# Kernel tuning notes

Measured on AMD Instinct MI355X. Metric: run time of the kernel, lower is better.

## Reference

```python
import jax, jax.numpy as jnp
import numpy as np

B, N, M = 4, 1024, 2048
D, H, HD, L, V = 768, 6, 128, 3, 4096
PEH = 64
FF = 4 * D
TEMP0 = 15.5


def _rms(x, w):
    return x * jax.lax.rsqrt(jnp.mean(x * x, axis=-1, keepdims=True) + 1e-8) * w


def _l2(x):
    n = jnp.sqrt(jnp.sum(x * x, axis=-1, keepdims=True))
    return x / jnp.maximum(n, 1e-12)


def setup_inputs():
    key = jax.random.key(0)
    it = iter(jax.random.split(key, 32))

    def rn(shape, s=0.02):
        return jax.random.normal(next(it), shape, jnp.float32) * s

    inp = {}
    inp['tokens'] = jax.random.randint(next(it), (B, N), 0, V)
    inp['acoustic'] = jax.random.normal(next(it), (B, M, D), jnp.float32)
    inp['embed'] = rn((V, D))
    inp['pe_freq'] = rn((PEH // 2,), 1.0)
    inp['pe_w'] = rn((PEH, D))
    inp['pe_b'] = jnp.zeros((D,), jnp.float32)
    inp['dpb_w0'] = rn((1, 64), 0.5)
    inp['dpb_b0'] = jnp.zeros((64,), jnp.float32)
    inp['dpb_w1'] = rn((64, 64), 0.1)
    inp['dpb_b1'] = jnp.zeros((64,), jnp.float32)
    inp['dpb_w2'] = rn((64, H), 0.1)
    inp['dpb_b2'] = jnp.zeros((H,), jnp.float32)
    inp['acoustic_norm_w'] = jnp.ones((D,), jnp.float32)
    inp['norm1'] = jnp.ones((L, D), jnp.float32)
    inp['norm2'] = jnp.ones((L, D), jnp.float32)
    inp['norm3'] = jnp.ones((L, D), jnp.float32)
    inp['sa_qkv'] = rn((L, D, 3 * H * HD))
    inp['sa_out'] = rn((L, H * HD, D))
    inp['temp'] = jnp.full((L,), TEMP0, jnp.float32)
    inp['ca_q'] = rn((L, D, H * HD))
    inp['ca_kv'] = rn((L, D, 2 * H * HD))
    inp['ca_out'] = rn((L, H * HD, D))
    inp['ff_w1'] = rn((L, D, FF))
    inp['ff_w2'] = rn((L, FF, D))
    inp['final_norm_w'] = jnp.ones((D,), jnp.float32)
    inp['out_w'] = rn((D, V))
    inp['out_b'] = jnp.zeros((V,), jnp.float32)
    return inp


def reference(tokens, acoustic, embed, pe_freq, pe_w, pe_b, dpb_w0, dpb_b0, dpb_w1, dpb_b1, dpb_w2, dpb_b2, acoustic_norm_w, norm1, norm2, norm3, sa_qkv, sa_out, temp, ca_q, ca_kv, ca_out, ff_w1, ff_w2, final_norm_w, out_w, out_b):
    x = embed[tokens]  # [B,N,D]
    # learnable fourier positional encoding (hidden_dim=64)
    p = jnp.arange(N, dtype=jnp.float32)[:, None]
    feat = jnp.concatenate([jnp.cos(p * pe_freq), jnp.sin(p * pe_freq)], axis=-1) / jnp.sqrt(jnp.float32(PEH))
    x = x + (feat @ pe_w + pe_b)

    # DynamicPositionBias: MLP over relative distance -> [H,N,N]
    dist = jnp.arange(-(N - 1), N, dtype=jnp.float32)[:, None]  # [2N-1,1]
    hmlp = jax.nn.silu(dist @ dpb_w0 + dpb_b0)
    hmlp = jax.nn.silu(hmlp @ dpb_w1 + dpb_b1)
    table = hmlp @ dpb_w2 + dpb_b2  # [2N-1, H]
    i = jnp.arange(N)
    rel = i[None, :] - i[:, None] + (N - 1)  # [N,N]
    pos_bias = jnp.transpose(table[rel], (2, 0, 1))  # [H,N,N]
    causal = i[None, :] > i[:, None]  # True where key index > query index
    neg = -jnp.finfo(jnp.float32).max

    xkv = _rms(acoustic, acoustic_norm_w)  # acoustic_norm applied once

    for l in range(L):
        # --- cosine-sim causal self-attention with temperature + pos bias ---
        hx = _rms(x, norm1[l])
        qkv = (hx @ sa_qkv[l]).reshape(B, N, H, HD, 3)  # 'b n (h d qkv)'
        q = jnp.transpose(qkv[..., 0], (0, 2, 1, 3))  # [B,H,N,HD]
        k = jnp.transpose(qkv[..., 1], (0, 2, 1, 3))
        v = jnp.transpose(qkv[..., 2], (0, 2, 1, 3))
        q, k = _l2(q), _l2(k)
        dots = jnp.einsum('bhid,bhjd->bhij', q, k) * temp[l] + pos_bias
        dots = jnp.where(causal, neg, dots)
        attn = jax.nn.softmax(dots, axis=-1)
        o = jnp.einsum('bhij,bhjd->bhid', attn, v)
        o = jnp.transpose(o, (0, 2, 1, 3)).reshape(B, N, H * HD)
        x = x + o @ sa_out[l]

        # --- cross attention to acoustic features (flash-attn math, scale 1/sqrt(d)) ---
        hx = _rms(x, norm2[l])
        q = (hx @ ca_q[l]).reshape(B, N, H, HD)
        kv = (xkv @ ca_kv[l]).reshape(B, M, H, HD, 2)  # 'b n (h d kv)'
        k, v = kv[..., 0], kv[..., 1]
        dots = jnp.einsum('bihd,bjhd->bhij', q, k) / jnp.sqrt(jnp.float32(HD))
        attn = jax.nn.softmax(dots, axis=-1)
        o = jnp.einsum('bhij,bjhd->bihd', attn, v).reshape(B, N, H * HD)
        x = x + o @ ca_out[l]

        # --- feed-forward: linear -> gelu -> linear ---
        hx = _rms(x, norm3[l])
        x = x + jax.nn.gelu(hx @ ff_w1[l], approximate=True) @ ff_w2[l]

    logits = _rms(x, final_norm_w) @ out_w + out_b  # [B,N,V]
    return logits
```

## Files before the change

kernel.cpp:

```cpp
#include <hip/hip_runtime.h>
#include <hip/hip_bf16.h>
#include <math.h>
#include <stddef.h>

#define Bc 4
#define Nc 1024
#define Mc 2048
#define Dc 768
#define Hc 6
#define HDc 128
#define Lc 3
#define Vc 4096
#define FFc 3072

typedef short bf16x8 __attribute__((ext_vector_type(8)));
typedef float f32x4 __attribute__((ext_vector_type(4)));
typedef ushort usx4 __attribute__((ext_vector_type(4)));

__device__ __forceinline__ float gelu_tanh(float x) {
    float x3 = x * x * x;
    return 0.5f * x * (1.0f + tanhf(0.7978845608028654f * (x + 0.044715f * x3)));
}
__device__ __forceinline__ float silu_f(float x) {
    return x / (1.0f + expf(-x));
}
__device__ __forceinline__ ushort f2bf(float x) {
    unsigned u = __float_as_uint(x);
    unsigned r = (u + 0x7fffu + ((u >> 16) & 1u)) >> 16;
    return (ushort)r;
}
__device__ __forceinline__ float bf2f(ushort u) {
    return __uint_as_float(((unsigned)u) << 16);
}
__device__ __forceinline__ void gl2lds16(const ushort* g, ushort* l) {
    __builtin_amdgcn_global_load_lds(
        (const __attribute__((address_space(1))) unsigned int*)(g),
        (__attribute__((address_space(3))) unsigned int*)(l),
        16, 0, 0);
}
__device__ __forceinline__ int xcd_swz(int bid, int nwg) {
    int q = nwg >> 3, r = nwg & 7;
    int xcd = bid & 7, i = bid >> 3;
    return (xcd < r ? xcd * (q + 1) : r * (q + 1) + (xcd - r) * q) + i;
}

__global__ __launch_bounds__(256) void pos_pe_kernel(
    const float* __restrict__ freq, const float* __restrict__ pe_w,
    const float* __restrict__ pe_b, float* __restrict__ pos)
{
    int n = blockIdx.x;
    __shared__ float feat[64];
    int tid = threadIdx.x;
    if (tid < 64) {
        float f;
        if (tid < 32) f = cosf((float)n * freq[tid]);
        else          f = sinf((float)n * freq[tid - 32]);
        feat[tid] = f * 0.125f;
    }
    __syncthreads();
    for (int d = tid; d < Dc; d += 256) {
        float s = pe_b[d];
#pragma unroll
        for (int h = 0; h < 64; ++h) s += feat[h] * pe_w[h * Dc + d];
        pos[(size_t)n * Dc + d] = s;
    }
}

__global__ __launch_bounds__(256) void embed_kernel(
    const int* __restrict__ tokens, const float* __restrict__ embed_w,
    const float* __restrict__ pos, float* __restrict__ x)
{
    size_t idx = (size_t)blockIdx.x * 256 + threadIdx.x;
    if (idx >= (size_t)Bc * Nc * Dc) return;
    int d  = (int)(idx % Dc);
    size_t bn = idx / Dc;
    int n  = (int)(bn % Nc);
    int tok = tokens[bn];
    x[idx] = embed_w[(size_t)tok * Dc + d] + pos[(size_t)n * Dc + d];
}

__global__ __launch_bounds__(64) void dpb_kernel(
    const float* __restrict__ w0, const float* __restrict__ b0,
    const float* __restrict__ w1, const float* __restrict__ b1,
    const float* __restrict__ w2, const float* __restrict__ b2,
    float* __restrict__ table)
{
    int r = blockIdx.x;
    int j = threadIdx.x;
    float dist = (float)r - (float)(Nc - 1);
    __shared__ float s0[64], s1[64];
    s0[j] = silu_f(dist * w0[j] + b0[j]);
    __syncthreads();
    float a = b1[j];
#pragma unroll 8
    for (int k = 0; k < 64; ++k) a += s0[k] * w1[k * 64 + j];
    s1[j] = silu_f(a);
    __syncthreads();
    if (j < Hc) {
        float t = b2[j];
#pragma unroll 8
        for (int k = 0; k < 64; ++k) t += s1[k] * w2[k * Hc + j];
        table[(size_t)r * Hc + j] = t;
    }
}

__global__ __launch_bounds__(256) void rms_kernel(
    const float* __restrict__ in, const float* __restrict__ w,
    ushort* __restrict__ out)
{
    size_t row = blockIdx.x;
    const float* rp = in + row * Dc;
    ushort* op = out + row * Dc;
    int tid = threadIdx.x;
    float4 v = make_float4(0.f, 0.f, 0.f, 0.f);
    float s = 0.f;
    int d4 = tid << 2;
    if (tid < 192) {
        v = *(const float4*)&rp[d4];
        s = v.x * v.x + v.y * v.y + v.z * v.z + v.w * v.w;
    }
    __shared__ float red[256];
    red[tid] = s;
    __syncthreads();
    for (int o = 128; o > 0; o >>= 1) {
        if (tid < o) red[tid] += red[tid + o];
        __syncthreads();
    }
    float rs = rsqrtf(red[0] * (1.0f / Dc) + 1e-8f);
    if (tid < 192) {
        float4 wv = *(const float4*)&w[d4];
        usx4 pk;
        pk.x = f2bf(v.x * rs * wv.x); pk.y = f2bf(v.y * rs * wv.y);
        pk.z = f2bf(v.z * rs * wv.z); pk.w = f2bf(v.w * rs * wv.w);
        *(usx4*)&op[d4] = pk;
    }
}

__global__ __launch_bounds__(256) void rms_reduce_kernel(
    float* __restrict__ x, const float* __restrict__ P, int nsplit, size_t MN,
    const float* __restrict__ w, ushort* __restrict__ out)
{
    size_t row = blockIdx.x;
    float* xp = x + row * Dc;
    ushort* op = out + row * Dc;
    int tid = threadIdx.x;
    int d4 = tid << 2;
    float4 v = make_float4(0.f, 0.f, 0.f, 0.f);
    float s = 0.f;
    if (tid < 192) {
        v = *(const float4*)&xp[d4];
        for (int z = 0; z < nsplit; ++z) {
            float4 p = *(const float4*)&P[(size_t)z * MN + row * Dc + d4];
            v.x += p.x; v.y += p.y; v.z += p.z; v.w += p.w;
        }
        *(float4*)&xp[d4] = v;
        s = v.x * v.x + v.y * v.y + v.z * v.z + v.w * v.w;
    }
    __shared__ float red[256];
    red[tid] = s;
    __syncthreads();
    for (int o = 128; o > 0; o >>= 1) {
        if (tid < o) red[tid] += red[tid + o];
        __syncthreads();
    }
    float rs = rsqrtf(red[0] * (1.0f / Dc) + 1e-8f);
    if (tid < 192) {
        float4 wv = *(const float4*)&w[d4];
        usx4 pk;
        pk.x = f2bf(v.x * rs * wv.x); pk.y = f2bf(v.y * rs * wv.y);
        pk.z = f2bf(v.z * rs * wv.z); pk.w = f2bf(v.w * rs * wv.w);
        *(usx4*)&op[d4] = pk;
    }
}

__global__ __launch_bounds__(256) void wt_kernel(
    const float* __restrict__ in, ushort* __restrict__ out, int K_, int N_)
{
    int n0 = blockIdx.x << 6, k0 = blockIdx.y << 6;
    __shared__ ushort t[64][65];
    int tid = threadIdx.x;
    int r = tid >> 4, c4 = (tid & 15) << 2;
    for (int rr = r; rr < 64; rr += 16) {
        float4 v = *(const float4*)&in[(size_t)(k0 + rr) * N_ + n0 + c4];
        t[rr][c4]     = f2bf(v.x);
        t[rr][c4 + 1] = f2bf(v.y);
        t[rr][c4 + 2] = f2bf(v.z);
        t[rr][c4 + 3] = f2bf(v.w);
    }
    __syncthreads();
    int nr = tid >> 2, cw = (tid & 3) << 4;
    ushort tmp[16];
#pragma unroll
    for (int j = 0; j < 16; ++j) tmp[j] = t[cw + j][nr];
#pragma unroll
    for (int s = 0; s < 2; ++s)
        *(bf16x8*)&out[(size_t)(n0 + nr) * K_ + k0 + cw + (s << 3)] =
            *(const bf16x8*)&tmp[s << 3];
}

__global__ __launch_bounds__(512) void gemm_bf16_kernel(
    const ushort* __restrict__ A, const ushort* __restrict__ Bt,
    const float* __restrict__ bias, const float* __restrict__ res,
    float* __restrict__ Cf, ushort* __restrict__ Cb,
    int M_, int N_, int K_, int act, int ksplit)
{
    __shared__ __align__(16) ushort sraw[2 * 2 * 8 * 512];
    ushort* As = sraw;
    ushort* Bs = sraw + 2 * 8 * 512;

    int nwg = gridDim.x * gridDim.y;
    int swz = xcd_swz(blockIdx.y * gridDim.x + blockIdx.x, nwg);
    int n0 = (swz % gridDim.x) << 7;
    int m0 = (swz / gridDim.x) << 7;

    int tid = threadIdx.x;
    int wave = tid >> 6, lane = tid & 63;
    int li = lane & 15, lq = lane >> 4;
    int wm = (wave >> 2) << 6;
    int wn = (wave & 3) << 5;

    int kchunk = K_ / ksplit;
    int kbeg = blockIdx.z * kchunk;
    int niter = kchunk >> 5;

    f32x4 acc[4][2];
#pragma unroll
    for (int i = 0; i < 4; ++i)
#pragma unroll
        for (int j = 0; j < 2; ++j) {
            acc[i][j][0] = 0.f; acc[i][j][1] = 0.f;
            acc[i][j][2] = 0.f; acc[i][j][3] = 0.f;
        }

    auto stage = [&](int buf, int k0) {
        const ushort* ga = A  + (size_t)(m0 + (wave << 4) + li) * K_ + k0 + (lq << 3);
        const ushort* gb = Bt + (size_t)(n0 + (wave << 4) + li) * K_ + k0 + (lq << 3);
        gl2lds16(ga, &As[(buf << 12) + (wave << 9)]);
        gl2lds16(gb, &Bs[(buf << 12) + (wave << 9)]);
    };

    stage(0, kbeg);
    __syncthreads();

    for (int it = 0; it < niter; ++it) {
        int cur = it & 1;
        if (it + 1 < niter) stage(cur ^ 1, kbeg + ((it + 1) << 5));
        bf16x8 af[4], bfr[2];
#pragma unroll
        for (int t = 0; t < 4; ++t)
            af[t]  = *(const bf16x8*)&As[(cur << 12) + (((wm >> 4) + t) << 9) + (lane << 3)];
#pragma unroll
        for (int t = 0; t < 2; ++t)
            bfr[t] = *(const bf16x8*)&Bs[(cur << 12) + (((wn >> 4) + t) << 9) + (lane << 3)];
#pragma unroll
        for (int mt = 0; mt < 4; ++mt)
#pragma unroll
            for (int nt = 0; nt < 2; ++nt)
                acc[mt][nt] = __builtin_amdgcn_mfma_f32_16x16x32_bf16(
                    af[mt], bfr[nt], acc[mt][nt], 0, 0, 0);
        __syncthreads();
    }

    float* lt = (float*)sraw;
    float* dstF = Cf;
    if (ksplit > 1) dstF = Cf + (size_t)blockIdx.z * M_ * N_;

#pragma unroll
    for (int half = 0; half < 2; ++half) {
        __syncthreads();
        if ((wm >> 6) == half) {
#pragma unroll
            for (int mt = 0; mt < 4; ++mt) {
#pragma unroll
                for (int r = 0; r < 4; ++r) {
                    int lrow = (mt << 4) + (lq << 2) + r;
                    int grow = m0 + (half << 6) + lrow;
#pragma unroll
                    for (int nt = 0; nt < 2; ++nt) {
                        int col = wn + (nt << 4) + li;
                        float v = acc[mt][nt][r];
                        if (ksplit == 1) {
                            int gcol = n0 + col;
                            if (bias) v += bias[gcol];
                            if (act == 1) v = gelu_tanh(v);
                            if (res) v += res[(size_t)grow * N_ + gcol];
                        }
                        lt[(lrow << 7) + col] = v;
                    }
                }
            }
        }
        __syncthreads();
        if (Cb) {
            int lrow = tid >> 4;
            int c8 = (tid & 15) << 3;
#pragma unroll
            for (int p = 0; p < 2; ++p) {
                int row = (p << 5) + lrow;
                f32x4 a = *(const f32x4*)&lt[(row << 7) + c8];
                f32x4 b = *(const f32x4*)&lt[(row << 7) + c8 + 4];
                union { bf16x8 v; ushort u[8]; } pk;
#pragma unroll
                for (int j = 0; j < 4; ++j) {
                    pk.u[j] = f2bf(a[j]);
                    pk.u[4 + j] = f2bf(b[j]);
                }
                int grow = m0 + (half << 6) + row;
                *(bf16x8*)&Cb[(size_t)grow * N_ + n0 + c8] = pk.v;
            }
        } else {
            int lrow = tid >> 5;
            int c4 = (tid & 31) << 2;
#pragma unroll
            for (int p = 0; p < 4; ++p) {
                int row = (p << 4) + lrow;
                f32x4 a = *(const f32x4*)&lt[(row << 7) + c4];
                int grow = m0 + (half << 6) + row;
                *(f32x4*)&dstF[(size_t)grow * N_ + n0 + c4] = a;
            }
        }
    }
}

__global__ __launch_bounds__(128) void unpack_sa_kernel(
    const ushort* __restrict__ qkv, ushort* __restrict__ qo,
    ushort* __restrict__ ko, ushort* __restrict__ vo)
{
    int bid = blockIdx.x;
    int h = bid % Hc;
    int bn = bid / Hc;
    int b = bn / Nc, n = bn % Nc;
    int d = threadIdx.x;
    size_t base = (size_t)bn * (3 * Hc * HDc) + (size_t)(h * HDc + d) * 3;
    float q = bf2f(qkv[base]), k = bf2f(qkv[base + 1]);
    ushort v = qkv[base + 2];
    __shared__ float rq[128], rk[128];
    rq[d] = q * q; rk[d] = k * k;
    __syncthreads();
    for (int o = 64; o > 0; o >>= 1) {
        if (d < o) { rq[d] += rq[d + o]; rk[d] += rk[d + o]; }
        __syncthreads();
    }
    float qn = fmaxf(sqrtf(rq[0]), 1e-12f);
    float kn = fmaxf(sqrtf(rk[0]), 1e-12f);
    size_t oidx = (((size_t)(b * Hc + h) * Nc) + n) * HDc + d;
    qo[oidx] = f2bf(q / qn);
    ko[oidx] = f2bf(k / kn);
    vo[oidx] = v;
}

__global__ __launch_bounds__(256) void unpack_caq_red_kernel(
    const float* __restrict__ P, ushort* __restrict__ qo)
{
    size_t idx = (size_t)blockIdx.x * 256 + threadIdx.x;
    if (idx >= (size_t)Bc * Hc * Nc * HDc) return;
    int d = (int)(idx & (HDc - 1));
    size_t t = idx >> 7;
    int n = (int)(t % Nc); t /= Nc;
    int h = (int)(t % Hc); int b = (int)(t / Hc);
    const size_t MNq = (size_t)Bc * Nc * (Hc * HDc);
    size_t src = ((size_t)(b * Nc + n)) * (Hc * HDc) + h * HDc + d;
    qo[idx] = f2bf(P[src] + P[MNq + src]);
}

__global__ __launch_bounds__(256) void unpack_cakv_kernel(
    const ushort* __restrict__ in, ushort* __restrict__ ko, ushort* __restrict__ vo)
{
    size_t idx = (size_t)blockIdx.x * 256 + threadIdx.x;
    if (idx >= (size_t)Bc * Hc * Mc * HDc) return;
    int d = (int)(idx & (HDc - 1));
    size_t t = idx >> 7;
    int m = (int)(t % Mc); t /= Mc;
    int h = (int)(t % Hc); int b = (int)(t / Hc);
    size_t src = ((size_t)(b * Mc + m)) * (2 * Hc * HDc) + (size_t)(h * HDc + d) * 2;
    ko[idx] = in[src];
    vo[idx] = in[src + 1];
}

__global__ __launch_bounds__(256) void transpose_kernel(
    const ushort* __restrict__ in, ushort* __restrict__ out, int R)
{
    int bh = blockIdx.z;
    int r0 = blockIdx.x << 6, d0 = blockIdx.y << 6;
    const ushort* ip = in + (size_t)bh * R * HDc;
    ushort* op = out + (size_t)bh * HDc * R;
    __shared__ ushort tile[64][66];
    int t = threadIdx.x;
    int lr = t >> 5, lc = (t & 31) << 1;
    for (int rr = lr; rr < 64; rr += 8) {
        ushort2 v = *(const ushort2*)&ip[(size_t)(r0 + rr) * HDc + d0 + lc];
        tile[rr][lc] = v.x; tile[rr][lc + 1] = v.y;
    }
    __syncthreads();
    for (int dd = lr; dd < 64; dd += 8) {
        ushort2 v;
        v.x = tile[lc][dd]; v.y = tile[lc + 1][dd];
        *(ushort2*)&op[(size_t)(d0 + dd) * R + r0 + lc] = v;
    }
}

__global__ __launch_bounds__(256) void attn_mfma_kernel(
    const ushort* __restrict__ Qg, const ushort* __restrict__ Kg,
    const ushort* __restrict__ VTg, ushort* __restrict__ O,
    int NQ, int NK, float scale_const, const float* __restrict__ scale_ptr,
    const float* __restrict__ bias_table, int causal)
{
    int qtiles = NQ >> 6;
    int bid = xcd_swz(blockIdx.x, gridDim.x);
    int qt = bid % qtiles;
    int bh = bid / qtiles;
    int h = bh % Hc, b = bh / Hc;
    int q0 = qt << 6;

    const ushort* Qb = Qg + (size_t)bh * NQ * HDc;
    const ushort* Kb = Kg + (size_t)bh * NK * HDc;
    const ushort* Vb = VTg + (size_t)bh * HDc * NK;

    float scale = scale_const * (scale_ptr ? scale_ptr[0] : 1.0f);

    __shared__ __align__(16) ushort Ks[2][16 * 512];
    __shared__ __align__(16) ushort Vs[2][16 * 512];
    __shared__ __align__(16) ushort Ps[4][16][72];
    __shared__ float bias_s[2][128];

    int tid = threadIdx.x;
    int wave = tid >> 6, lane = tid & 63;
    int li = lane & 15, lq = lane >> 4;
    int qrel = (wave << 4) + li;

    bf16x8 qfrag[4];
    {
        const ushort* qrow = Qb + (size_t)(q0 + qrel) * HDc + (lq << 3);
#pragma unroll
        for (int kt = 0; kt < 4; ++kt)
            qfrag[kt] = *(const bf16x8*)&qrow[kt << 5];
    }

    f32x4 oacc[8];
#pragma unroll
    for (int i = 0; i < 8; ++i) { oacc[i][0] = 0.f; oacc[i][1] = 0.f; oacc[i][2] = 0.f; oacc[i][3] = 0.f; }
    float m_run = -INFINITY, l_run = 0.f;

    auto stage_kv = [&](int buf, int jt) {
        int j0 = jt << 6;
#pragma unroll
        for (int i = 0; i < 4; ++i) {
            int f = (wave << 2) + i;
            int mt = f >> 2, kt = f & 3;
            const ushort* gk = Kb + (size_t)(j0 + (mt << 4) + li) * HDc + (kt << 5) + (lq << 3);
            gl2lds16(gk, &Ks[buf][f << 9]);
            int dt = f >> 1, s = f & 1;
            const ushort* gv = Vb + (size_t)((dt << 4) + li) * NK + j0 + (s << 5) + (lq << 3);
            gl2lds16(gv, &Vs[buf][f << 9]);
        }
        if (bias_table && tid < 127)
            bias_s[buf][tid] = bias_table[(size_t)(j0 - q0 - 63 + Nc - 1 + tid) * Hc + h];
    };

    int jt_end = causal ? (q0 >> 6) + 1 : (NK >> 6);

    stage_kv(0, 0);
    __syncthreads();

    for (int jt = 0; jt < jt_end; ++jt) {
        int cur = jt & 1;
        if (jt + 1 < jt_end) stage_kv(cur ^ 1, jt + 1);
        int j0 = jt << 6;

        f32x4 sacc[4];
#pragma unroll
        for (int mt = 0; mt < 4; ++mt) {
            f32x4 s; s[0] = 0.f; s[1] = 0.f; s[2] = 0.f; s[3] = 0.f;
#pragma unroll
            for (int kt = 0; kt < 4; ++kt) {
                bf16x8 kf = *(const bf16x8*)&Ks[cur][(((mt << 2) + kt) << 9) + (lane << 3)];
                s = __builtin_amdgcn_mfma_f32_16x16x32_bf16(kf, qfrag[kt], s, 0, 0, 0);
            }
            sacc[mt] = s;
        }

        float sv[4][4];
        float mtile = -INFINITY;
#pragma unroll
        for (int mt = 0; mt < 4; ++mt)
#pragma unroll
            for (int r = 0; r < 4; ++r) {
                int jrel = (mt << 4) + (lq << 2) + r;
                float sx = sacc[mt][r] * scale;
                if (bias_table) sx += bias_s[cur][jrel - qrel + 63];
                if (causal && (j0 + jrel) > (q0 + qrel)) sx = -INFINITY;
                sv[mt][r] = sx;
                mtile = fmaxf(mtile, sx);
            }
        mtile = fmaxf(mtile, __shfl_xor(mtile, 16));
        mtile = fmaxf(mtile, __shfl_xor(mtile, 32));
        float m_new = fmaxf(m_run, mtile);
        float alpha = __expf(m_run - m_new);
        m_run = m_new;
        float ps = 0.f;
#pragma unroll
        for (int mt = 0; mt < 4; ++mt)
#pragma unroll
            for (int r = 0; r < 4; ++r) {
                float p = __expf(sv[mt][r] - m_new);
                sv[mt][r] = p;
                ps += p;
            }
        ps += __shfl_xor(ps, 16);
        ps += __shfl_xor(ps, 32);
        l_run = l_run * alpha + ps;

#pragma unroll
        for (int mt = 0; mt < 4; ++mt) {
            usx4 pk;
            pk.x = f2bf(sv[mt][0]); pk.y = f2bf(sv[mt][1]);
            pk.z = f2bf(sv[mt][2]); pk.w = f2bf(sv[mt][3]);
            *(usx4*)&Ps[wave][li][(mt << 4) + (lq << 2)] = pk;
        }

        float ar[4];
#pragma unroll
        for (int r = 0; r < 4; ++r) ar[r] = __shfl(alpha, (lq << 2) + r);
#pragma unroll
        for (int dt = 0; dt < 8; ++dt)
#pragma unroll
            for (int r = 0; r < 4; ++r) oacc[dt][r] *= ar[r];

        bf16x8 pf0 = *(const bf16x8*)&Ps[wave][li][(lq << 3)];
        bf16x8 pf1 = *(const bf16x8*)&Ps[wave][li][32 + (lq << 3)];
#pragma unroll
        for (int dt = 0; dt < 8; ++dt) {
            bf16x8 v0 = *(const bf16x8*)&Vs[cur][(((dt << 1) + 0) << 9) + (lane << 3)];
            bf16x8 v1 = *(const bf16x8*)&Vs[cur][(((dt << 1) + 1) << 9) + (lane << 3)];
            oacc[dt] = __builtin_amdgcn_mfma_f32_16x16x32_bf16(pf0, v0, oacc[dt], 0, 0, 0);
            oacc[dt] = __builtin_amdgcn_mfma_f32_16x16x32_bf16(pf1, v1, oacc[dt], 0, 0, 0);
        }
        __syncthreads();
    }

#pragma unroll
    for (int r = 0; r < 4; ++r) {
        float linv = 1.0f / __shfl(l_run, (lq << 2) + r);
        int gq = q0 + (wave << 4) + (lq << 2) + r;
        ushort* op = O + ((size_t)(b * NQ + gq)) * (Hc * HDc) + h * HDc;
#pragma unroll
        for (int dt = 0; dt < 8; ++dt)
            op[(dt << 4) + li] = f2bf(oacc[dt][r] * linv);
    }
}

static inline void launch_gemm(const ushort* A, const ushort* Bt, const float* bias,
                               const float* res, float* Cf, ushort* Cb,
                               int M_, int N_, int K_, int act, int ksplit,
                               hipStream_t s)
{
    dim3 g(N_ / 128, M_ / 128, ksplit);
    hipLaunchKernelGGL(gemm_bf16_kernel, g, dim3(512), 0, s,
                       A, Bt, bias, res, Cf, Cb, M_, N_, K_, act, ksplit);
}

extern "C" void kernel_launch(void* const* d_in, const int* in_sizes, int n_in,
                              void* d_out, int out_size, void* d_ws, size_t ws_size,
                              hipStream_t stream)
{
    const int*   tokens   = (const int*)  d_in[0];
    const float* acoustic = (const float*)d_in[1];
    const float* embed_w  = (const float*)d_in[2];
    const float* pe_freq  = (const float*)d_in[3];
    const float* pe_w     = (const float*)d_in[4];
    const float* pe_b     = (const float*)d_in[5];
    const float* dpb_w0   = (const float*)d_in[6];
    const float* dpb_b0   = (const float*)d_in[7];
    const float* dpb_w1   = (const float*)d_in[8];
    const float* dpb_b1   = (const float*)d_in[9];
    const float* dpb_w2   = (const float*)d_in[10];
    const float* dpb_b2   = (const float*)d_in[11];
    const float* ac_nw    = (const float*)d_in[12];
    const float* norm1    = (const float*)d_in[13];
    const float* norm2    = (const float*)d_in[14];
    const float* norm3    = (const float*)d_in[15];
    const float* sa_qkv   = (const float*)d_in[16];
    const float* sa_out_w = (const float*)d_in[17];
    const float* temp     = (const float*)d_in[18];
    const float* ca_q_w   = (const float*)d_in[19];
    const float* ca_kv_w  = (const float*)d_in[20];
    const float* ca_out_w = (const float*)d_in[21];
    const float* ff_w1    = (const float*)d_in[22];
    const float* ff_w2    = (const float*)d_in[23];
    const float* fin_nw   = (const float*)d_in[24];
    const float* out_w    = (const float*)d_in[25];
    const float* out_b    = (const float*)d_in[26];
    float* out = (float*)d_out;

    const size_t SZ_X   = (size_t)Bc * Nc * Dc;
    const size_t SZ_POS = (size_t)Nc * Dc;
    const size_t SZ_TAB = 16384;
    const size_t SZ_XKV = (size_t)Bc * Mc * Dc;
    const size_t SZ_BIG = (size_t)Bc * Nc * FFc;
    const size_t SZ_QH  = (size_t)Bc * Hc * Nc * HDc;
    const size_t SZ_KH  = (size_t)Bc * Hc * Mc * HDc;

    float* ws = (float*)d_ws;
    float* x     = ws;
    float* pos   = x + SZ_X;
    float* table = pos + SZ_POS;
    ushort* hx    = (ushort*)(table + SZ_TAB);
    ushort* xkvb  = hx + SZ_X;
    ushort* attnO = xkvb + SZ_XKV;
    ushort* bigBb = attnO + SZ_X;
    ushort* qb    = bigBb + SZ_BIG;
    ushort* kb    = qb + SZ_QH;
    ushort* vb    = kb + SZ_KH;
    ushort* vTb   = vb + SZ_KH;
    ushort* wT    = vTb + SZ_KH;

    const size_t W_QKV = (size_t)Dc * 3 * Hc * HDc;
    const size_t W_O   = (size_t)Hc * HDc * Dc;
    const size_t W_CKV = (size_t)Dc * 2 * Hc * HDc;
    const size_t W_F   = (size_t)Dc * FFc;
    const size_t W_LAYER = W_QKV + 3 * W_O + W_CKV + 2 * W_F;
    ushort* outWT = wT + 3 * W_LAYER;

    float* Pq = (float*)qb;
    float* Pk = (float*)kb;
    const size_t MN = (size_t)Bc * Nc * Dc;

    const float CA_SCALE = 0.08838834764831843f;

    for (int l = 0; l < Lc; ++l) {
        ushort* wl = wT + (size_t)l * W_LAYER;
        ushort* qkvT = wl;
        ushort* soT  = qkvT + W_QKV;
        ushort* cqT  = soT + W_O;
        ushort* ckvT = cqT + W_O;
        ushort* coT  = ckvT + W_CKV;
        ushort* f1T  = coT + W_O;
        ushort* f2T  = f1T + W_F;
        hipLaunchKernelGGL(wt_kernel, dim3(3 * Hc * HDc / 64, Dc / 64), dim3(256), 0, stream,
                           sa_qkv + (size_t)l * W_QKV, qkvT, Dc, 3 * Hc * HDc);
        hipLaunchKernelGGL(wt_kernel, dim3(Dc / 64, Hc * HDc / 64), dim3(256), 0, stream,
                           sa_out_w + (size_t)l * W_O, soT, Hc * HDc, Dc);
        hipLaunchKernelGGL(wt_kernel, dim3(Hc * HDc / 64, Dc / 64), dim3(256), 0, stream,
                           ca_q_w + (size_t)l * W_O, cqT, Dc, Hc * HDc);
        hipLaunchKernelGGL(wt_kernel, dim3(2 * Hc * HDc / 64, Dc / 64), dim3(256), 0, stream,
                           ca_kv_w + (size_t)l * W_CKV, ckvT, Dc, 2 * Hc * HDc);
        hipLaunchKernelGGL(wt_kernel, dim3(Dc / 64, Hc * HDc / 64), dim3(256), 0, stream,
                           ca_out_w + (size_t)l * W_O, coT, Hc * HDc, Dc);
        hipLaunchKernelGGL(wt_kernel, dim3(FFc / 64, Dc / 64), dim3(256), 0, stream,
                           ff_w1 + (size_t)l * W_F, f1T, Dc, FFc);
        hipLaunchKernelGGL(wt_kernel, dim3(Dc / 64, FFc / 64), dim3(256), 0, stream,
                           ff_w2 + (size_t)l * W_F, f2T, FFc, Dc);
    }
    hipLaunchKernelGGL(wt_kernel, dim3(Vc / 64, Dc / 64), dim3(256), 0, stream,
                       out_w, outWT, Dc, Vc);

    hipLaunchKernelGGL(pos_pe_kernel, dim3(Nc), dim3(256), 0, stream,
                       pe_freq, pe_w, pe_b, pos);
    hipLaunchKernelGGL(embed_kernel, dim3((unsigned)((SZ_X + 255) / 256)), dim3(256), 0, stream,
                       tokens, embed_w, pos, x);
    hipLaunchKernelGGL(dpb_kernel, dim3(2 * Nc - 1), dim3(64), 0, stream,
                       dpb_w0, dpb_b0, dpb_w1, dpb_b1, dpb_w2, dpb_b2, table);
    hipLaunchKernelGGL(rms_kernel, dim3(Bc * Mc), dim3(256), 0, stream,
                       acoustic, ac_nw, xkvb);

    for (int l = 0; l < Lc; ++l) {
        const float* n1 = norm1 + (size_t)l * Dc;
        const float* n2 = norm2 + (size_t)l * Dc;
        const float* n3 = norm3 + (size_t)l * Dc;
        ushort* wl = wT + (size_t)l * W_LAYER;
        ushort* qkvT = wl;
        ushort* soT  = qkvT + W_QKV;
        ushort* cqT  = soT + W_O;
        ushort* ckvT = cqT + W_O;
        ushort* coT  = ckvT + W_CKV;
        ushort* f1T  = coT + W_O;
        ushort* f2T  = f1T + W_F;

        if (l == 0)
            hipLaunchKernelGGL(rms_kernel, dim3(Bc * Nc), dim3(256), 0, stream, x, n1, hx);
        else
            hipLaunchKernelGGL(rms_reduce_kernel, dim3(Bc * Nc), dim3(256), 0, stream,
                               x, Pq, 3, MN, n1, hx);
        launch_gemm(hx, qkvT, nullptr, nullptr, nullptr, bigBb,
                    Bc * Nc, 3 * Hc * HDc, Dc, 0, 1, stream);
        hipLaunchKernelGGL(unpack_sa_kernel, dim3(Bc * Nc * Hc), dim3(128), 0, stream,
                           bigBb, qb, kb, vb);
        hipLaunchKernelGGL(transpose_kernel, dim3(Nc / 64, 2, Bc * Hc), dim3(256), 0, stream,
                           vb, vTb, Nc);
        hipLaunchKernelGGL(attn_mfma_kernel, dim3(Bc * Hc * (Nc / 64)), dim3(256), 0, stream,
                           qb, kb, vTb, attnO, Nc, Nc, 1.0f, temp + l, table, 1);
        launch_gemm(attnO, soT, nullptr, nullptr, Pq, nullptr,
                    Bc * Nc, Dc, Hc * HDc, 0, 3, stream);
        hipLaunchKernelGGL(rms_reduce_kernel, dim3(Bc * Nc), dim3(256), 0, stream,
                           x, Pq, 3, MN, n2, hx);

        launch_gemm(hx, cqT, nullptr, nullptr, Pk, nullptr,
                    Bc * Nc, Hc * HDc, Dc, 0, 2, stream);
        hipLaunchKernelGGL(unpack_caq_red_kernel, dim3((unsigned)((SZ_QH + 255) / 256)),
                           dim3(256), 0, stream, Pk, qb);
        launch_gemm(xkvb, ckvT, nullptr, nullptr, nullptr, bigBb,
                    Bc * Mc, 2 * Hc * HDc, Dc, 0, 1, stream);
        hipLaunchKernelGGL(unpack_cakv_kernel, dim3((unsigned)((SZ_KH + 255) / 256)), dim3(256),
                           0, stream, bigBb, kb, vb);
        hipLaunchKernelGGL(transpose_kernel, dim3(Mc / 64, 2, Bc * Hc), dim3(256), 0, stream,
                           vb, vTb, Mc);
        hipLaunchKernelGGL(attn_mfma_kernel, dim3(Bc * Hc * (Nc / 64)), dim3(256), 0, stream,
                           qb, kb, vTb, attnO, Nc, Mc, CA_SCALE, nullptr, nullptr, 0);
        launch_gemm(attnO, coT, nullptr, nullptr, Pq, nullptr,
                    Bc * Nc, Dc, Hc * HDc, 0, 3, stream);
        hipLaunchKernelGGL(rms_reduce_kernel, dim3(Bc * Nc), dim3(256), 0, stream,
                           x, Pq, 3, MN, n3, hx);

        launch_gemm(hx, f1T, nullptr, nullptr, nullptr, bigBb,
                    Bc * Nc, FFc, Dc, 1, 1, stream);
        launch_gemm(bigBb, f2T, nullptr, nullptr, Pq, nullptr,
                    Bc * Nc, Dc, FFc, 0, 3, stream);
    }

    hipLaunchKernelGGL(rms_reduce_kernel, dim3(Bc * Nc), dim3(256), 0, stream,
                       x, Pq, 3, MN, fin_nw, hx);
    launch_gemm(hx, outWT, out_b, nullptr, out, nullptr,
                Bc * Nc, Vc, Dc, 0, 1, stream);
}
```

Before: 1.822 ms.

## Split attention over two KV partitions and merge with a combine kernel

The self- and cross-attention kernels now split each query tile's key/value range into two strided halves, launching twice as many blocks. Each half writes unnormalised fp32 partial outputs plus its running max and sum, and a new combine kernel merges the two halves with log-sum-exp weighting into the bf16 output. The aim is better CU occupancy and load balance, since the original 384-block grid underfills the device and causal tiles have uneven work. The cost is an extra fp32 partial write and read, one extra launch per attention call, and reuse of the existing bigBb and pos buffers as scratch.

Measured after the change: 1.876 ms. 1.03x slower.

```diff
diff --git a/kernel.cpp b/kernel.cpp
--- a/kernel.cpp
+++ b/kernel.cpp
@@ -403,12 +403,16 @@
     const ushort* __restrict__ Qg, const ushort* __restrict__ Kg,
     const ushort* __restrict__ VTg, ushort* __restrict__ O,
     int NQ, int NK, float scale_const, const float* __restrict__ scale_ptr,
-    const float* __restrict__ bias_table, int causal)
+    const float* __restrict__ bias_table, int causal,
+    int nsplit, float* __restrict__ Opart, float* __restrict__ ml)
 {
     int qtiles = NQ >> 6;
     int bid = xcd_swz(blockIdx.x, gridDim.x);
-    int qt = bid % qtiles;
-    int bh = bid / qtiles;
+    int slab = gridDim.x / nsplit;
+    int z = bid / slab;
+    int r0b = bid % slab;
+    int qt = r0b % qtiles;
+    int bh = r0b / qtiles;
     int h = bh % Hc, b = bh / Hc;
     int q0 = qt << 6;
 
@@ -459,12 +463,12 @@
 
     int jt_end = causal ? (q0 >> 6) + 1 : (NK >> 6);
 
-    stage_kv(0, 0);
-    __syncthreads();
-
-    for (int jt = 0; jt < jt_end; ++jt) {
-        int cur = jt & 1;
-        if (jt + 1 < jt_end) stage_kv(cur ^ 1, jt + 1);
+    if (z < jt_end) stage_kv(0, z);
+    __syncthreads();
+
+    int cur = 0;
+    for (int jt = z; jt < jt_end; jt += nsplit) {
+        if (jt + nsplit < jt_end) stage_kv(cur ^ 1, jt + nsplit);
         int j0 = jt << 6;
 
         f32x4 sacc[4];
@@ -536,17 +540,66 @@
             oacc[dt] = __builtin_amdgcn_mfma_f32_16x16x32_bf16(pf1, v1, oacc[dt], 0, 0, 0);
         }
         __syncthreads();
-    }
-
-#pragma unroll
-    for (int r = 0; r < 4; ++r) {
-        float linv = 1.0f / __shfl(l_run, (lq << 2) + r);
-        int gq = q0 + (wave << 4) + (lq << 2) + r;
-        ushort* op = O + ((size_t)(b * NQ + gq)) * (Hc * HDc) + h * HDc;
-#pragma unroll
-        for (int dt = 0; dt < 8; ++dt)
-            op[(dt << 4) + li] = f2bf(oacc[dt][r] * linv);
-    }
+        cur ^= 1;
+    }
+
+    if (nsplit == 1) {
+#pragma unroll
+        for (int r = 0; r < 4; ++r) {
+            float linv = 1.0f / __shfl(l_run, (lq << 2) + r);
+            int gq = q0 + (wave << 4) + (lq << 2) + r;
+            ushort* op = O + ((size_t)(b * NQ + gq)) * (Hc * HDc) + h * HDc;
+#pragma unroll
+            for (int dt = 0; dt < 8; ++dt)
+                op[(dt << 4) + li] = f2bf(oacc[dt][r] * linv);
+        }
+    } else {
+        const size_t SZX = (size_t)Bc * NQ * Hc * HDc;
+        float* Opz = Opart + (size_t)z * SZX;
+#pragma unroll
+        for (int r = 0; r < 4; ++r) {
+            int gq = q0 + (wave << 4) + (lq << 2) + r;
+            float* op = Opz + ((size_t)(b * NQ + gq)) * (Hc * HDc) + h * HDc;
+#pragma unroll
+            for (int dt = 0; dt < 8; ++dt)
+                op[(dt << 4) + li] = oacc[dt][r];
+        }
+        if (lq == 0) {
+            size_t mi = (((size_t)z * (Bc * Hc) + bh) * NQ + (q0 + (wave << 4) + li)) * 2;
+            ml[mi] = m_run;
+            ml[mi + 1] = l_run;
+        }
+    }
+}
+
+__global__ __launch_bounds__(256) void attn_combine_kernel(
+    const float* __restrict__ Op, const float* __restrict__ ml,
+    ushort* __restrict__ O, int NQ)
+{
+    int bn = blockIdx.x;
+    int tid = threadIdx.x;
+    if (tid >= 192) return;
+    int b = bn / NQ, n = bn % NQ;
+    int d4 = tid << 2;
+    int h = d4 >> 7;
+    int bh = b * Hc + h;
+    const size_t SZX = (size_t)Bc * NQ * Hc * HDc;
+    size_t roff = (size_t)bn * (Hc * HDc) + d4;
+    size_t mi0 = ((size_t)bh * NQ + n) * 2;
+    size_t mi1 = (((size_t)(Bc * Hc) + bh) * NQ + n) * 2;
+    float m0 = ml[mi0], l0 = ml[mi0 + 1];
+    float m1 = ml[mi1], l1 = ml[mi1 + 1];
+    float m = fmaxf(m0, m1);
+    float w0 = __expf(m0 - m), w1 = __expf(m1 - m);
+    float dinv = 1.0f / (l0 * w0 + l1 * w1);
+    float4 a = *(const float4*)&Op[roff];
+    float4 c = *(const float4*)&Op[SZX + roff];
+    usx4 pk;
+    pk.x = f2bf((a.x * w0 + c.x * w1) * dinv);
+    pk.y = f2bf((a.y * w0 + c.y * w1) * dinv);
+    pk.z = f2bf((a.z * w0 + c.z * w1) * dinv);
+    pk.w = f2bf((a.w * w0 + c.w * w1) * dinv);
+    *(usx4*)&O[roff] = pk;
 }
 
 static inline void launch_gemm(const ushort* A, const ushort* Bt, const float* bias,
@@ -625,6 +678,9 @@
     float* Pk = (float*)kb;
     const size_t MN = (size_t)Bc * Nc * Dc;
 
+    float* OpA = (float*)bigBb;
+    float* mlA = pos;
+
     const float CA_SCALE = 0.08838834764831843f;
 
     for (int l = 0; l < Lc; ++l) {
@@ -663,6 +719,8 @@
     hipLaunchKernelGGL(rms_kernel, dim3(Bc * Mc), dim3(256), 0, stream,
                        acoustic, ac_nw, xkvb);
 
+    const int ATTN_GRID = Bc * Hc * (Nc / 64) * 2;
+
     for (int l = 0; l < Lc; ++l) {
         const float* n1 = norm1 + (size_t)l * Dc;
         const float* n2 = norm2 + (size_t)l * Dc;
@@ -687,8 +745,11 @@
                            bigBb, qb, kb, vb);
         hipLaunchKernelGGL(transpose_kernel, dim3(Nc / 64, 2, Bc * Hc), dim3(256), 0, stream,
                            vb, vTb, Nc);
-        hipLaunchKernelGGL(attn_mfma_kernel, dim3(Bc * Hc * (Nc / 64)), dim3(256), 0, stream,
-                           qb, kb, vTb, attnO, Nc, Nc, 1.0f, temp + l, table, 1);
+        hipLaunchKernelGGL(attn_mfma_kernel, dim3(ATTN_GRID), dim3(256), 0, stream,
+                           qb, kb, vTb, attnO, Nc, Nc, 1.0f, temp + l, table, 1,
+                           2, OpA, mlA);
+        hipLaunchKernelGGL(attn_combine_kernel, dim3(Bc * Nc), dim3(256), 0, stream,
+                           OpA, mlA, attnO, Nc);
         launch_gemm(attnO, soT, nullptr, nullptr, Pq, nullptr,
                     Bc * Nc, Dc, Hc * HDc, 0, 3, stream);
         hipLaunchKernelGGL(rms_reduce_kernel, dim3(Bc * Nc), dim3(256), 0, stream,
@@ -704,8 +765,11 @@
                            0, stream, bigBb, kb, vb);
         hipLaunchKernelGGL(transpose_kernel, dim3(Mc / 64, 2, Bc * Hc), dim3(256), 0, stream,
                            vb, vTb, Mc);
-        hipLaunchKernelGGL(attn_mfma_kernel, dim3(Bc * Hc * (Nc / 64)), dim3(256), 0, stream,
-                           qb, kb, vTb, attnO, Nc, Mc, CA_SCALE, nullptr, nullptr, 0);
+        hipLaunchKernelGGL(attn_mfma_kernel, dim3(ATTN_GRID), dim3(256), 0, stream,
+                           qb, kb, vTb, attnO, Nc, Mc, CA_SCALE, nullptr, nullptr, 0,
+                           2, OpA, mlA);
+        hipLaunchKernelGGL(attn_combine_kernel, dim3(Bc * Nc), dim3(256), 0, stream,
+                           OpA, mlA, attnO, Nc);
         launch_gemm(attnO, coT, nullptr, nullptr, Pq, nullptr,
                     Bc * Nc, Dc, Hc * HDc, 0, 3, stream);
         hipLaunchKernelGGL(rms_reduce_kernel, dim3(Bc * Nc), dim3(256), 0, stream,
```
